# Kernel tuning notes

Measured on AMD Instinct MI355X. Metric: run time of the kernel, lower is better.

## Reference

```python
import jax, jax.numpy as jnp
import numpy as np

FEAT = 2048
NUM_CLASSES = 751
EPS = 1e-5


def setup_inputs() -> dict:
    key = jax.random.key(0)
    k1, k2, k3 = jax.random.split(key, 3)
    probe_x = jax.random.normal(k1, (64, FEAT), dtype=jnp.float32)
    gallery_x = jax.random.normal(k2, (256, FEAT), dtype=jnp.float32)
    # BatchNorm1d affine params (PyTorch init: gamma=1, beta=0)
    bn_gamma = jnp.ones((FEAT,), dtype=jnp.float32)
    bn_beta = jnp.zeros((FEAT,), dtype=jnp.float32)
    # classifier: weight ~ N(0, 0.001), bias = 0
    W = jax.random.normal(k3, (NUM_CLASSES, FEAT), dtype=jnp.float32) * 0.001
    b = jnp.zeros((NUM_CLASSES,), dtype=jnp.float32)
    return {"probe_x": probe_x, "gallery_x": gallery_x,
            "bn_gamma": bn_gamma, "bn_beta": bn_beta, "W": W, "b": b}


def reference(probe_x, gallery_x, bn_gamma, bn_beta, W, b):
    n_probe, feat = probe_x.shape
    n_gallery = gallery_x.shape[0]
    # broadcast squared difference: [Np, Ng, F]
    diff = jnp.square(probe_x[:, None, :] - gallery_x[None, :, :])
    d = diff.reshape(n_probe * n_gallery, feat)
    # BatchNorm1d in training mode: biased batch statistics over the batch dim
    mean = jnp.mean(d, axis=0)
    var = jnp.mean(jnp.square(d - mean), axis=0)
    bn = (d - mean) * (bn_gamma / jnp.sqrt(var + EPS)) + bn_beta
    # Linear classifier
    cls = jnp.einsum('nf,cf->nc', bn, W) + b
    return cls.reshape(n_probe, n_gallery, -1)
```

## Files before the change

### kernel.cpp

```cpp
#include <hip/hip_runtime.h>
#include <hip/hip_bf16.h>
#include <hip/hip_fp16.h>

#define FEAT 2048
#define NCLS 751
#define NPAD 768
#define NPRB 64
#define NGAL 256
#define WSCALE 256.0f

typedef _Float16 f16x8 __attribute__((ext_vector_type(8)));
typedef float f32x4 __attribute__((ext_vector_type(4)));

__device__ __forceinline__ unsigned short f2h_u(float x) {
  union { _Float16 h; unsigned short u; } v;
  v.h = (_Float16)x;
  return v.u;
}

__global__ void stats_kernel(const float* __restrict__ P, const float* __restrict__ G,
                             const float* __restrict__ gamma, const float* __restrict__ beta,
                             float* __restrict__ st) {
  int fx = threadIdx.x & 31, ry = threadIdx.x >> 5;
  int f = blockIdx.x * 32 + fx;
  float a1 = 0, a2 = 0, a3 = 0, a4 = 0;
  for (int r = ry; r < NPRB; r += 8) {
    float x = P[r * FEAT + f], x2 = x * x;
    a1 += x; a2 += x2; a3 += x2 * x; a4 += x2 * x2;
  }
  float b1 = 0, b2 = 0, b3 = 0, b4 = 0;
  for (int r = ry; r < NGAL; r += 8) {
    float x = G[r * FEAT + f], x2 = x * x;
    b1 += x; b2 += x2; b3 += x2 * x; b4 += x2 * x2;
  }
  __shared__ float red[8][8][32];
  float vals[8] = {a1, a2, a3, a4, b1, b2, b3, b4};
#pragma unroll
  for (int m = 0; m < 8; ++m) red[m][ry][fx] = vals[m];
  __syncthreads();
  if (ry == 0) {
    float mm[8];
#pragma unroll
    for (int m = 0; m < 8; ++m) {
      float sum = 0.f;
#pragma unroll
      for (int r = 0; r < 8; ++r) sum += red[m][r][fx];
      mm[m] = sum;
    }
    float M1p = mm[0] * (1.f / NPRB), M2p = mm[1] * (1.f / NPRB);
    float M3p = mm[2] * (1.f / NPRB), M4p = mm[3] * (1.f / NPRB);
    float M1g = mm[4] * (1.f / NGAL), M2g = mm[5] * (1.f / NGAL);
    float M3g = mm[6] * (1.f / NGAL), M4g = mm[7] * (1.f / NGAL);
    float mean = M2p - 2.f * M1p * M1g + M2g;
    float Ed2 = M4p - 4.f * M3p * M1g + 6.f * M2p * M2g - 4.f * M1p * M3g + M4g;
    float var = Ed2 - mean * mean;
    float sv = gamma[f] / sqrtf(var + 1e-5f);
    st[f] = sv;
    st[FEAT + f] = beta[f] - mean * sv;
  }
}

__global__ void prepw_kernel(const float* __restrict__ W, const float* __restrict__ b,
                             const float* __restrict__ st,
                             unsigned short* __restrict__ Wf, float* __restrict__ bp) {
  const int nblk = blockIdx.x;
  const int t = threadIdx.x;
  const int row = t & 15;
  const int c = nblk * 16 + row;
  const int kcb = t >> 4;
  unsigned short* wbase = Wf + (size_t)nblk * 32768;
  float part = 0.f;
#pragma unroll 4
  for (int i = 0; i < 16; ++i) {
    int kc = i * 16 + kcb;
    int f = kc * 8;
    float4 w0 = make_float4(0.f, 0.f, 0.f, 0.f), w1 = w0;
    if (c < NCLS) {
      const float4* ws = (const float4*)(W + (size_t)c * FEAT + f);
      w0 = ws[0]; w1 = ws[1];
    }
    const float4* s4 = (const float4*)(st + f);
    float4 s0 = s4[0], s1 = s4[1];
    const float4* t4 = (const float4*)(st + FEAT + f);
    float4 t0 = t4[0], t1 = t4[1];
    uint4 u;
    u.x = (unsigned int)f2h_u(w0.x * s0.x * WSCALE) | ((unsigned int)f2h_u(w0.y * s0.y * WSCALE) << 16);
    u.y = (unsigned int)f2h_u(w0.z * s0.z * WSCALE) | ((unsigned int)f2h_u(w0.w * s0.w * WSCALE) << 16);
    u.z = (unsigned int)f2h_u(w1.x * s1.x * WSCALE) | ((unsigned int)f2h_u(w1.y * s1.y * WSCALE) << 16);
    u.w = (unsigned int)f2h_u(w1.z * s1.z * WSCALE) | ((unsigned int)f2h_u(w1.w * s1.w * WSCALE) << 16);
    *(uint4*)(wbase + (size_t)kc * 128 + row * 8) = u;
    part += t0.x * w0.x + t0.y * w0.y + t0.z * w0.z + t0.w * w0.w +
            t1.x * w1.x + t1.y * w1.y + t1.z * w1.z + t1.w * w1.w;
  }
  __shared__ float red[16][16];
  red[kcb][row] = part;
  __syncthreads();
  if (t < 16) {
    float sum = (nblk * 16 + t < NCLS) ? b[nblk * 16 + t] : 0.f;
#pragma unroll
    for (int j = 0; j < 16; ++j) sum += red[j][t];
    bp[nblk * 16 + t] = sum;
  }
}

__global__ void agen_kernel(const float* __restrict__ P, const float* __restrict__ G,
                            unsigned short* __restrict__ A) {
  int n = blockIdx.x;
  int p = n >> 8, g = n & 255;
  int f = threadIdx.x * 8;
  const float4* p4 = (const float4*)(P + (size_t)p * FEAT + f);
  const float4* g4 = (const float4*)(G + (size_t)g * FEAT + f);
  float4 pa = p4[0], pb = p4[1];
  float4 ga = g4[0], gb = g4[1];
  float d0 = pa.x - ga.x, d1 = pa.y - ga.y, d2 = pa.z - ga.z, d3 = pa.w - ga.w;
  float d4 = pb.x - gb.x, d5 = pb.y - gb.y, d6 = pb.z - gb.z, d7 = pb.w - gb.w;
  uint4 u;
  u.x = (unsigned int)f2h_u(d0 * d0) | ((unsigned int)f2h_u(d1 * d1) << 16);
  u.y = (unsigned int)f2h_u(d2 * d2) | ((unsigned int)f2h_u(d3 * d3) << 16);
  u.z = (unsigned int)f2h_u(d4 * d4) | ((unsigned int)f2h_u(d5 * d5) << 16);
  u.w = (unsigned int)f2h_u(d6 * d6) | ((unsigned int)f2h_u(d7 * d7) << 16);
  *(uint4*)(A + (size_t)n * FEAT + f) = u;
}

__global__ __launch_bounds__(256, 3)
void gemm_mat_kernel(const unsigned short* __restrict__ A,
                     const unsigned short* __restrict__ Wf,
                     const float* __restrict__ bp, float* __restrict__ out) {
  __shared__ unsigned short As[128 * 64];

  const int tid = threadIdx.x;
  const int lane = tid & 63, wave = tid >> 6;
  const int mtile = blockIdx.x, ntile = blockIdx.y;

  const int srow = tid >> 3;
  const int sch = (tid & 7) ^ (srow & 7);
  const unsigned short* ag = A + (size_t)(mtile * 128 + srow) * FEAT + sch * 8;
  char* alds = (char*)As + wave * 1024;

  f32x4 acc[4][4];
#pragma unroll
  for (int mi = 0; mi < 4; ++mi)
#pragma unroll
    for (int ni = 0; ni < 4; ++ni) acc[mi][ni] = (f32x4){0.f, 0.f, 0.f, 0.f};

  const int wm = (wave & 1) * 64, wn = (wave >> 1) * 64;
  const int frow = lane & 15, fsw = lane & 7, fk = lane >> 4;

  const unsigned short* wfbase =
      Wf + ((size_t)ntile * 8 + (wn >> 4)) * 32768 + lane * 8;

  f16x8 bfa[2][4], bfb[2][4];
#pragma unroll
  for (int kk = 0; kk < 2; ++kk)
#pragma unroll
    for (int ni = 0; ni < 4; ++ni)
      bfa[kk][ni] = *(const f16x8*)(wfbase + (size_t)ni * 32768 + kk * 512);

#define STAGE_A(K0)                                                              \
  do {                                                                           \
    __syncthreads();                                                             \
    _Pragma("unroll") for (int j = 0; j < 4; ++j)                                \
        __builtin_amdgcn_global_load_lds(                                        \
            (const __attribute__((address_space(1))) void*)(ag + (K0) +          \
                                                            (size_t)j * 32 * FEAT), \
            (__attribute__((address_space(3))) void*)(alds + j * 4096), 16, 0, 0);
#define PREFETCH_B(DST, K0)                                                      \
    _Pragma("unroll") for (int kk = 0; kk < 2; ++kk)                             \
      _Pragma("unroll") for (int ni = 0; ni < 4; ++ni)                           \
        DST[kk][ni] = *(const f16x8*)(wfbase + (size_t)ni * 32768 + (K0)*16 + kk * 512);
#define COMPUTE(SRC)                                                             \
    __syncthreads();                                                             \
    _Pragma("unroll") for (int kk = 0; kk < 2; ++kk) {                           \
      const int slot = (kk * 4 + fk) ^ fsw;                                      \
      f16x8 af[4];                                                               \
      _Pragma("unroll") for (int mi = 0; mi < 4; ++mi)                           \
          af[mi] = *(const f16x8*)(As + (wm + mi * 16 + frow) * 64 + slot * 8);  \
      _Pragma("unroll") for (int mi = 0; mi < 4; ++mi)                           \
        _Pragma("unroll") for (int ni = 0; ni < 4; ++ni)                         \
            acc[mi][ni] = __builtin_amdgcn_mfma_f32_16x16x32_f16(                \
                af[mi], SRC[kk][ni], acc[mi][ni], 0, 0, 0);                      \
    }                                                                            \
  } while (0)

  for (int k0 = 0; k0 < FEAT; k0 += 128) {
    STAGE_A(k0)
    PREFETCH_B(bfb, k0 + 64)
    COMPUTE(bfa);
    STAGE_A(k0 + 64)
    if (k0 + 128 < FEAT) { PREFETCH_B(bfa, k0 + 128) }
    COMPUTE(bfb);
  }
#undef STAGE_A
#undef PREFETCH_B
#undef COMPUTE

  const int col0 = ntile * 128 + wn + (lane & 15);
  const int row0 = mtile * 128 + wm + ((lane >> 4) << 2);
#pragma unroll
  for (int ni = 0; ni < 4; ++ni) {
    int col = col0 + ni * 16;
    if (col >= NCLS) continue;
    float bv = bp[col];
#pragma unroll
    for (int mi = 0; mi < 4; ++mi) {
      int row = row0 + mi * 16;
#pragma unroll
      for (int r = 0; r < 4; ++r)
        out[(size_t)(row + r) * NCLS + col] = acc[mi][ni][r] * (1.0f / WSCALE) + bv;
    }
  }
}

extern "C" void kernel_launch(void* const* d_in, const int* in_sizes, int n_in,
                              void* d_out, int out_size, void* d_ws, size_t ws_size,
                              hipStream_t stream) {
  const float* P = (const float*)d_in[0];
  const float* G = (const float*)d_in[1];
  const float* gamma = (const float*)d_in[2];
  const float* beta = (const float*)d_in[3];
  const float* W = (const float*)d_in[4];
  const float* b = (const float*)d_in[5];
  float* out = (float*)d_out;

  float* st = (float*)d_ws;
  float* bp = st + 2 * FEAT;
  unsigned short* Wf = (unsigned short*)(bp + NPAD);
  unsigned short* A = Wf + (size_t)48 * 32768;

  hipLaunchKernelGGL(agen_kernel, dim3(NPRB * NGAL), dim3(256), 0, stream, P, G, A);
  hipLaunchKernelGGL(stats_kernel, dim3(64), dim3(256), 0, stream, P, G, gamma, beta, st);
  hipLaunchKernelGGL(prepw_kernel, dim3(48), dim3(256), 0, stream, W, b, st, Wf, bp);
  hipLaunchKernelGGL(gemm_mat_kernel, dim3(128, 6), dim3(256), 0, stream, A, Wf, bp, out);
}
```

Measured before the change: 190.6 us.

## Pre-swizzle A into MFMA fragment layout and load both operands directly from global

The A-generation kernel now writes squared differences in the same 16-row fragment-packed layout already used for W, so each lane can fetch a ready MFMA operand with one 16-byte load. The GEMM drops its LDS staging, barriers and global_load_lds path and instead double-buffers A and B fragments in registers from global memory. The grid is also transposed so blocks sharing an A tile launch next to each other, which helps L2 reuse. The cost is that A is read by each wave without LDS sharing, so global/L2 traffic for A rises, and the A-generation writes become strided.

Result: slower. 218.4 us (+14.6%).

```diff
diff --git a/kernel.cpp b/kernel.cpp
--- a/kernel.cpp
+++ b/kernel.cpp
@@ -105,37 +105,41 @@
 
 __global__ void agen_kernel(const float* __restrict__ P, const float* __restrict__ G,
                             unsigned short* __restrict__ A) {
-  int n = blockIdx.x;
-  int p = n >> 8, g = n & 255;
-  int f = threadIdx.x * 8;
-  const float4* p4 = (const float4*)(P + (size_t)p * FEAT + f);
-  const float4* g4 = (const float4*)(G + (size_t)g * FEAT + f);
-  float4 pa = p4[0], pb = p4[1];
-  float4 ga = g4[0], gb = g4[1];
-  float d0 = pa.x - ga.x, d1 = pa.y - ga.y, d2 = pa.z - ga.z, d3 = pa.w - ga.w;
-  float d4 = pb.x - gb.x, d5 = pb.y - gb.y, d6 = pb.z - gb.z, d7 = pb.w - gb.w;
-  uint4 u;
-  u.x = (unsigned int)f2h_u(d0 * d0) | ((unsigned int)f2h_u(d1 * d1) << 16);
-  u.y = (unsigned int)f2h_u(d2 * d2) | ((unsigned int)f2h_u(d3 * d3) << 16);
-  u.z = (unsigned int)f2h_u(d4 * d4) | ((unsigned int)f2h_u(d5 * d5) << 16);
-  u.w = (unsigned int)f2h_u(d6 * d6) | ((unsigned int)f2h_u(d7 * d7) << 16);
-  *(uint4*)(A + (size_t)n * FEAT + f) = u;
+  const int mblk = blockIdx.x;
+  const int row = threadIdx.x & 15, kcb = threadIdx.x >> 4;
+  const int p = mblk >> 4;
+  const int g = (mblk & 15) * 16 + row;
+  unsigned short* abase = A + (size_t)mblk * 32768;
+#pragma unroll 4
+  for (int i = 0; i < 16; ++i) {
+    int kc = i * 16 + kcb;
+    int f = kc * 8;
+    const float4* p4 = (const float4*)(P + (size_t)p * FEAT + f);
+    const float4* g4 = (const float4*)(G + (size_t)g * FEAT + f);
+    float4 pa = p4[0], pb = p4[1];
+    float4 ga = g4[0], gb = g4[1];
+    float d0 = pa.x - ga.x, d1 = pa.y - ga.y, d2 = pa.z - ga.z, d3 = pa.w - ga.w;
+    float d4 = pb.x - gb.x, d5 = pb.y - gb.y, d6 = pb.z - gb.z, d7 = pb.w - gb.w;
+    uint4 u;
+    u.x = (unsigned int)f2h_u(d0 * d0) | ((unsigned int)f2h_u(d1 * d1) << 16);
+    u.y = (unsigned int)f2h_u(d2 * d2) | ((unsigned int)f2h_u(d3 * d3) << 16);
+    u.z = (unsigned int)f2h_u(d4 * d4) | ((unsigned int)f2h_u(d5 * d5) << 16);
+    u.w = (unsigned int)f2h_u(d6 * d6) | ((unsigned int)f2h_u(d7 * d7) << 16);
+    *(uint4*)(abase + (size_t)kc * 128 + row * 8) = u;
+  }
 }
 
 __global__ __launch_bounds__(256, 3)
-void gemm_mat_kernel(const unsigned short* __restrict__ A,
-                     const unsigned short* __restrict__ Wf,
-                     const float* __restrict__ bp, float* __restrict__ out) {
-  __shared__ unsigned short As[128 * 64];
-
+void gemm_kernel(const unsigned short* __restrict__ A,
+                 const unsigned short* __restrict__ Wf,
+                 const float* __restrict__ bp, float* __restrict__ out) {
   const int tid = threadIdx.x;
   const int lane = tid & 63, wave = tid >> 6;
-  const int mtile = blockIdx.x, ntile = blockIdx.y;
-
-  const int srow = tid >> 3;
-  const int sch = (tid & 7) ^ (srow & 7);
-  const unsigned short* ag = A + (size_t)(mtile * 128 + srow) * FEAT + sch * 8;
-  char* alds = (char*)As + wave * 1024;
+  const int ntile = blockIdx.x, mtile = blockIdx.y;
+  const int wm = (wave & 1) * 64, wn = (wave >> 1) * 64;
+
+  const unsigned short* ab = A + ((size_t)mtile * 8 + (wm >> 4)) * 32768 + lane * 8;
+  const unsigned short* bb = Wf + ((size_t)ntile * 8 + (wn >> 4)) * 32768 + lane * 8;
 
   f32x4 acc[4][4];
 #pragma unroll
@@ -143,56 +147,30 @@
 #pragma unroll
     for (int ni = 0; ni < 4; ++ni) acc[mi][ni] = (f32x4){0.f, 0.f, 0.f, 0.f};
 
-  const int wm = (wave & 1) * 64, wn = (wave >> 1) * 64;
-  const int frow = lane & 15, fsw = lane & 7, fk = lane >> 4;
-
-  const unsigned short* wfbase =
-      Wf + ((size_t)ntile * 8 + (wn >> 4)) * 32768 + lane * 8;
-
-  f16x8 bfa[2][4], bfb[2][4];
-#pragma unroll
-  for (int kk = 0; kk < 2; ++kk)
-#pragma unroll
-    for (int ni = 0; ni < 4; ++ni)
-      bfa[kk][ni] = *(const f16x8*)(wfbase + (size_t)ni * 32768 + kk * 512);
-
-#define STAGE_A(K0)                                                              \
-  do {                                                                           \
-    __syncthreads();                                                             \
-    _Pragma("unroll") for (int j = 0; j < 4; ++j)                                \
-        __builtin_amdgcn_global_load_lds(                                        \
-            (const __attribute__((address_space(1))) void*)(ag + (K0) +          \
-                                                            (size_t)j * 32 * FEAT), \
-            (__attribute__((address_space(3))) void*)(alds + j * 4096), 16, 0, 0);
-#define PREFETCH_B(DST, K0)                                                      \
-    _Pragma("unroll") for (int kk = 0; kk < 2; ++kk)                             \
-      _Pragma("unroll") for (int ni = 0; ni < 4; ++ni)                           \
-        DST[kk][ni] = *(const f16x8*)(wfbase + (size_t)ni * 32768 + (K0)*16 + kk * 512);
-#define COMPUTE(SRC)                                                             \
-    __syncthreads();                                                             \
-    _Pragma("unroll") for (int kk = 0; kk < 2; ++kk) {                           \
-      const int slot = (kk * 4 + fk) ^ fsw;                                      \
-      f16x8 af[4];                                                               \
-      _Pragma("unroll") for (int mi = 0; mi < 4; ++mi)                           \
-          af[mi] = *(const f16x8*)(As + (wm + mi * 16 + frow) * 64 + slot * 8);  \
-      _Pragma("unroll") for (int mi = 0; mi < 4; ++mi)                           \
-        _Pragma("unroll") for (int ni = 0; ni < 4; ++ni)                         \
-            acc[mi][ni] = __builtin_amdgcn_mfma_f32_16x16x32_f16(                \
-                af[mi], SRC[kk][ni], acc[mi][ni], 0, 0, 0);                      \
-    }                                                                            \
-  } while (0)
-
-  for (int k0 = 0; k0 < FEAT; k0 += 128) {
-    STAGE_A(k0)
-    PREFETCH_B(bfb, k0 + 64)
-    COMPUTE(bfa);
-    STAGE_A(k0 + 64)
-    if (k0 + 128 < FEAT) { PREFETCH_B(bfa, k0 + 128) }
-    COMPUTE(bfb);
-  }
-#undef STAGE_A
-#undef PREFETCH_B
-#undef COMPUTE
+  f16x8 afa[4], bfa[4], afb[4], bfb[4];
+
+#define LD_A(DST, K0)                                                      \
+  _Pragma("unroll") for (int mi = 0; mi < 4; ++mi)                         \
+      DST[mi] = *(const f16x8*)(ab + (size_t)mi * 32768 + (K0) * 16);
+#define LD_B(DST, K0)                                                      \
+  _Pragma("unroll") for (int ni = 0; ni < 4; ++ni)                         \
+      DST[ni] = *(const f16x8*)(bb + (size_t)ni * 32768 + (K0) * 16);
+#define MM(AF, BF)                                                         \
+  _Pragma("unroll") for (int mi = 0; mi < 4; ++mi)                         \
+    _Pragma("unroll") for (int ni = 0; ni < 4; ++ni)                       \
+        acc[mi][ni] = __builtin_amdgcn_mfma_f32_16x16x32_f16(              \
+            AF[mi], BF[ni], acc[mi][ni], 0, 0, 0);
+
+  LD_A(afa, 0) LD_B(bfa, 0)
+  for (int k0 = 0; k0 < FEAT; k0 += 64) {
+    LD_A(afb, k0 + 32) LD_B(bfb, k0 + 32)
+    MM(afa, bfa)
+    if (k0 + 64 < FEAT) { LD_A(afa, k0 + 64) LD_B(bfa, k0 + 64) }
+    MM(afb, bfb)
+  }
+#undef LD_A
+#undef LD_B
+#undef MM
 
   const int col0 = ntile * 128 + wn + (lane & 15);
   const int row0 = mtile * 128 + wm + ((lane >> 4) << 2);
@@ -227,8 +205,8 @@
   unsigned short* Wf = (unsigned short*)(bp + NPAD);
   unsigned short* A = Wf + (size_t)48 * 32768;
 
-  hipLaunchKernelGGL(agen_kernel, dim3(NPRB * NGAL), dim3(256), 0, stream, P, G, A);
+  hipLaunchKernelGGL(agen_kernel, dim3(1024), dim3(256), 0, stream, P, G, A);
   hipLaunchKernelGGL(stats_kernel, dim3(64), dim3(256), 0, stream, P, G, gamma, beta, st);
   hipLaunchKernelGGL(prepw_kernel, dim3(48), dim3(256), 0, stream, W, b, st, Wf, bp);
-  hipLaunchKernelGGL(gemm_mat_kernel, dim3(128, 6), dim3(256), 0, stream, A, Wf, bp, out);
-}
+  hipLaunchKernelGGL(gemm_kernel, dim3(6, 128), dim3(256), 0, stream, A, Wf, bp, out);
+}
```
